# Optimization experiments

Hardware: AMD Instinct MI355X
Metric: run time of the kernel (lower is better)

Reference implementation:

```python
import jax, jax.numpy as jnp
import numpy as np

B, P, D = 64, 128, 128   # clouds, points per cloud, vec_dim
N = B * P                # 8192 nodes
EPS = 1e-5


def _complete_graph_edges():
    # knn_graph with k == total node count => complete graph per cloud (no self loops)
    i = np.arange(P)
    ii, jj = np.meshgrid(i, i, indexing='ij')
    m = ii != jj
    li, lj = ii[m], jj[m]                      # [P*(P-1)] local pairs
    off = (np.arange(B) * P)[:, None]          # cloud offsets
    src = (off + li[None, :]).reshape(-1)      # neighbor index
    dst = (off + lj[None, :]).reshape(-1)      # center index
    return jnp.asarray(src, jnp.int32), jnp.asarray(dst, jnp.int32)


def setup_inputs() -> dict:
    key = jax.random.key(0)
    ks = jax.random.split(key, 4)
    src, dst = _complete_graph_edges()
    return {
        'x': jax.random.normal(ks[0], (N, D), jnp.float32),
        'xyz': jax.random.normal(ks[1], (N, 3), jnp.float32),
        'W_xyz': jax.random.normal(ks[2], (3, D), jnp.float32) * 0.1,
        'bn_gamma': jnp.ones((D,), jnp.float32),
        'bn_beta': jnp.zeros((D,), jnp.float32),
        'W1': jax.random.normal(ks[3], (D, D), jnp.float32) * 0.05,
        'b1': jnp.zeros((D,), jnp.float32),
        'ln_gamma': jnp.ones((D,), jnp.float32),
        'ln_beta': jnp.zeros((D,), jnp.float32),
        'src': src,
        'dst': dst,
    }


def reference(x, xyz, W_xyz, bn_gamma, bn_beta, W1, b1, ln_gamma, ln_beta, src, dst):
    n = x.shape[0]
    rela_xyz = xyz[src] - xyz[dst]                         # [E, 3]
    rela_x = x[src] - x[dst]                               # [E, D]
    dist = jnp.sqrt(jnp.sum(rela_xyz * rela_xyz, axis=-1))  # [E]
    w = jnp.exp(-dist)[:, None]                            # [E, 1]

    # weighted linear + relu, pool by src (global_add_pool over node index)
    h1 = jax.nn.relu((w * rela_x) @ W1 + b1)               # [E, D]
    p1 = jax.ops.segment_sum(h1, src, num_segments=n)      # [N, D]
    mu = jnp.mean(p1, axis=-1, keepdims=True)
    var = jnp.var(p1, axis=-1, keepdims=True)
    x = x + ((p1 - mu) / jnp.sqrt(var + EPS)) * ln_gamma + ln_beta

    # xyz projection branch, BatchNorm1d (training-mode batch stats)
    h2 = jax.nn.relu(rela_xyz @ W_xyz)                     # [E, D]
    p2 = jax.ops.segment_sum(h2, src, num_segments=n)      # [N, D]
    bmu = jnp.mean(p2, axis=0)
    bvar = jnp.var(p2, axis=0)
    x = x + ((p2 - bmu) / jnp.sqrt(bvar + EPS)) * bn_gamma + bn_beta
    return x
```

## Files before the change

### kernel.cpp

```cpp
#include <hip/hip_runtime.h>
#include <stdint.h>

#define EPS 1e-5f
#define N_NODES 8192

typedef __attribute__((ext_vector_type(8))) short short8;
typedef __attribute__((ext_vector_type(4))) float floatx4;
typedef __attribute__((ext_vector_type(2))) float floatx2;
typedef __attribute__((ext_vector_type(4))) unsigned short ushortx4;

__device__ __forceinline__ unsigned short f2bf(float f) {
    uint32_t u = __float_as_uint(f);
    u += 0x7FFFu + ((u >> 16) & 1u);
    return (unsigned short)(u >> 16);
}

__global__ __launch_bounds__(256) void prep_kernel(
    const float* __restrict__ x, const float* __restrict__ W1,
    unsigned short* __restrict__ xb, unsigned short* __restrict__ w1t,
    float* __restrict__ stat_ws)
{
    const int bx = blockIdx.x, tid = threadIdx.x;
    if (bx < 1024) {
        const int base = bx * 1024 + tid * 4;
        floatx4 v = *(const floatx4*)(x + base);
        ushortx4 o = { f2bf(v[0]), f2bf(v[1]), f2bf(v[2]), f2bf(v[3]) };
        *(ushortx4*)(xb + base) = o;
    } else {
        const int b2 = bx - 1024;
        const int n = b2 * 8 + (tid >> 5);
        const int k = (tid & 31) * 4;
#pragma unroll
        for (int e = 0; e < 4; ++e)
            w1t[n * 128 + k + e] = f2bf(W1[(k + e) * 128 + n]);
        if (b2 == 0) {
            floatx4 z = {0.f, 0.f, 0.f, 0.f};
            *(floatx4*)(stat_ws + tid * 4) = z;
        }
    }
}

__global__ __launch_bounds__(64) void gemm_y_kernel(
    const unsigned short* __restrict__ xb, const unsigned short* __restrict__ w1t,
    float* __restrict__ y)
{
    const int lane = threadIdx.x;
    const int ml = lane & 15, q = lane >> 4;
    const int rb = blockIdx.x * 16;

    short8 afrag[4];
#pragma unroll
    for (int c = 0; c < 4; ++c)
        afrag[c] = *(const short8*)(xb + (rb + ml) * 128 + c * 32 + q * 8);

#pragma unroll
    for (int nt = 0; nt < 8; ++nt) {
        floatx4 acc = {0.f, 0.f, 0.f, 0.f};
        const int ncol = nt * 16 + ml;
#pragma unroll
        for (int c = 0; c < 4; ++c) {
            short8 b = *(const short8*)(w1t + ncol * 128 + c * 32 + q * 8);
            acc = __builtin_amdgcn_mfma_f32_16x16x32_bf16(afrag[c], b, acc, 0, 0, 0);
        }
#pragma unroll
        for (int r = 0; r < 4; ++r)
            y[(rb + q * 4 + r) * 128 + ncol] = acc[r];
    }
}

__global__ __launch_bounds__(256, 4) void cloud_main_kernel(
    const float* __restrict__ x, const float* __restrict__ xyz,
    const float* __restrict__ W_xyz, const float* __restrict__ b1,
    const float* __restrict__ ln_gamma, const float* __restrict__ ln_beta,
    const float* __restrict__ y_ws, float* __restrict__ p2_ws,
    float* __restrict__ stat_ws, float* __restrict__ out)
{
    __shared__ float s_xyz[512];
    __shared__ float s_w[1024];
    __shared__ float s_red[2048];
    __shared__ float s_p1[1088];
    __shared__ float s_bn[256];
    __shared__ float s_mu[8];
    __shared__ float s_rs[8];

    const int bx = blockIdx.x;
    const int c = bx & 63, s = bx >> 6;
    const int tid = threadIdx.x;
    const int d = tid & 127, h = tid >> 7;
    const int node0 = c * 128;
    const int i0 = s * 8;

    if (tid < 128) {
        const float* p = xyz + (node0 + tid) * 3;
        s_xyz[tid * 4 + 0] = p[0];
        s_xyz[tid * 4 + 1] = p[1];
        s_xyz[tid * 4 + 2] = p[2];
        s_xyz[tid * 4 + 3] = 0.f;
    }
    __syncthreads();

    for (int e = tid; e < 1024; e += 256) {
        const int j = e >> 3, ii = e & 7, ia = i0 + ii;
        float dx = s_xyz[ia * 4]     - s_xyz[j * 4];
        float dy = s_xyz[ia * 4 + 1] - s_xyz[j * 4 + 1];
        float dz = s_xyz[ia * 4 + 2] - s_xyz[j * 4 + 2];
        s_w[j * 8 + ii] = __expf(-sqrtf(dx * dx + dy * dy + dz * dz));
    }
    __syncthreads();

    const float w0 = W_xyz[d], w1c = W_xyz[128 + d], w2c = W_xyz[256 + d];
    const float b1d = b1[d];
    const floatx2 b1v = {b1d, b1d};
    const floatx2 zv2 = {0.f, 0.f};

    floatx2 yi[4], zi[4], a1[4], a2[4];
#pragma unroll
    for (int r = 0; r < 8; ++r) {
        const int ia = i0 + r;
        yi[r >> 1][r & 1] = y_ws[(node0 + ia) * 128 + d];
        zi[r >> 1][r & 1] = s_xyz[ia * 4] * w0 + s_xyz[ia * 4 + 1] * w1c
                          + s_xyz[ia * 4 + 2] * w2c;
        a1[r >> 1][r & 1] = 0.f;
        a2[r >> 1][r & 1] = 0.f;
    }

    const float* yrow = y_ws + (node0 + h * 64) * 128 + d;
    const float* wp = s_w + h * 64 * 8;
    const float* xp = s_xyz + h * 64 * 4;

#pragma unroll 4
    for (int j = 0; j < 64; ++j) {
        const float yj = yrow[j * 128];
        floatx4 xj = *(const floatx4*)(xp + j * 4);
        const float zj = xj[0] * w0 + xj[1] * w1c + xj[2] * w2c;
        floatx4 wa = *(const floatx4*)(wp + j * 8);
        floatx4 wb = *(const floatx4*)(wp + j * 8 + 4);
        const floatx2 yj2 = {yj, yj}, zj2 = {zj, zj};
        floatx2 wlo = {wa[0], wa[1]}, wmd = {wa[2], wa[3]};
        floatx2 wh0 = {wb[0], wb[1]}, wh1 = {wb[2], wb[3]};
        a1[0] += __builtin_elementwise_max(wlo * (yi[0] - yj2) + b1v, zv2);
        a1[1] += __builtin_elementwise_max(wmd * (yi[1] - yj2) + b1v, zv2);
        a1[2] += __builtin_elementwise_max(wh0 * (yi[2] - yj2) + b1v, zv2);
        a1[3] += __builtin_elementwise_max(wh1 * (yi[3] - yj2) + b1v, zv2);
        a2[0] += __builtin_elementwise_max(zi[0] - zj2, zv2);
        a2[1] += __builtin_elementwise_max(zi[1] - zj2, zv2);
        a2[2] += __builtin_elementwise_max(zi[2] - zj2, zv2);
        a2[3] += __builtin_elementwise_max(zi[3] - zj2, zv2);
    }
    __syncthreads();

    if (h == 1) {
#pragma unroll
        for (int r = 0; r < 8; ++r) {
            s_red[r * 128 + d]        = a1[r >> 1][r & 1];
            s_red[1024 + r * 128 + d] = a2[r >> 1][r & 1];
        }
    }
    __syncthreads();

    if (h == 0) {
        const float selfc = fmaxf(b1d, 0.f);
        float bs = 0.f, bq = 0.f;
#pragma unroll
        for (int r = 0; r < 8; ++r) {
            float v1 = a1[r >> 1][r & 1] + s_red[r * 128 + d] - selfc;
            float v2 = a2[r >> 1][r & 1] + s_red[1024 + r * 128 + d];
            a1[r >> 1][r & 1] = v1;
            a2[r >> 1][r & 1] = v2;
            s_p1[r * 136 + d] = v1;
            bs += v2;
            bq += v2 * v2;
        }
        s_bn[d] = bs;
        s_bn[128 + d] = bq;
    }
    __syncthreads();

    {
        const int ii = tid >> 5, sub = tid & 31;
        floatx4 v = *(const floatx4*)(s_p1 + ii * 136 + sub * 4);
        float ps = v[0] + v[1] + v[2] + v[3];
        float pq = v[0] * v[0] + v[1] * v[1] + v[2] * v[2] + v[3] * v[3];
#pragma unroll
        for (int m = 1; m < 32; m <<= 1) {
            ps += __shfl_xor(ps, m, 64);
            pq += __shfl_xor(pq, m, 64);
        }
        if (sub == 0) {
            float mu = ps * (1.f / 128.f);
            float var = pq * (1.f / 128.f) - mu * mu;
            s_mu[ii] = mu;
            s_rs[ii] = rsqrtf(var + EPS);
        }
    }
    if (tid < 128) {
        const int bank = (s & 3) * 256;
        atomicAdd(stat_ws + bank + d,       s_bn[d]);
        atomicAdd(stat_ws + bank + 128 + d, s_bn[128 + d]);
    }
    __syncthreads();

    if (h == 0) {
        const float lng = ln_gamma[d], lnb = ln_beta[d];
#pragma unroll
        for (int r = 0; r < 8; ++r) {
            const int gi = node0 + i0 + r;
            float o = x[gi * 128 + d] + (a1[r >> 1][r & 1] - s_mu[r]) * s_rs[r] * lng + lnb;
            out[gi * 128 + d] = o;
            p2_ws[gi * 128 + d] = a2[r >> 1][r & 1];
        }
    }
}

__global__ __launch_bounds__(256) void finalize_kernel(
    const float* __restrict__ p2_ws, const float* __restrict__ stat_ws,
    const float* __restrict__ bn_gamma, const float* __restrict__ bn_beta,
    float* __restrict__ out)
{
    __shared__ float sA[128], sB[128];
    const int tid = threadIdx.x;
    if (tid < 128) {
        float sm = 0.f, sq = 0.f;
#pragma unroll
        for (int b = 0; b < 4; ++b) {
            sm += stat_ws[b * 256 + tid];
            sq += stat_ws[b * 256 + 128 + tid];
        }
        float mu = sm * (1.f / 8192.f);
        float var = sq * (1.f / 8192.f) - mu * mu;
        float rs = rsqrtf(var + EPS);
        float A = rs * bn_gamma[tid];
        sA[tid] = A;
        sB[tid] = bn_beta[tid] - mu * A;
    }
    __syncthreads();
    const int base = (blockIdx.x * 256 + tid) * 4;
    const int d0 = base & 127;
    floatx4 p2 = *(const floatx4*)(p2_ws + base);
    floatx4 o  = *(const floatx4*)(out + base);
#pragma unroll
    for (int e = 0; e < 4; ++e)
        o[e] += p2[e] * sA[d0 + e] + sB[d0 + e];
    *(floatx4*)(out + base) = o;
}

extern "C" void kernel_launch(void* const* d_in, const int* in_sizes, int n_in,
                              void* d_out, int out_size, void* d_ws, size_t ws_size,
                              hipStream_t stream) {
    const float* x        = (const float*)d_in[0];
    const float* xyz      = (const float*)d_in[1];
    const float* W_xyz    = (const float*)d_in[2];
    const float* bn_gamma = (const float*)d_in[3];
    const float* bn_beta  = (const float*)d_in[4];
    const float* W1       = (const float*)d_in[5];
    const float* b1       = (const float*)d_in[6];
    const float* ln_gamma = (const float*)d_in[7];
    const float* ln_beta  = (const float*)d_in[8];
    float* out = (float*)d_out;

    float* y_ws    = (float*)d_ws;
    float* p2_ws   = y_ws + N_NODES * 128;
    float* stat_ws = p2_ws + N_NODES * 128;
    unsigned short* xb  = (unsigned short*)(stat_ws + 1024);
    unsigned short* w1t = xb + N_NODES * 128;

    prep_kernel<<<1040, 256, 0, stream>>>(x, W1, xb, w1t, stat_ws);
    gemm_y_kernel<<<512, 64, 0, stream>>>(xb, w1t, y_ws);
    cloud_main_kernel<<<1024, 256, 0, stream>>>(x, xyz, W_xyz, b1, ln_gamma, ln_beta,
                                                y_ws, p2_ws, stat_ws, out);
    finalize_kernel<<<1024, 256, 0, stream>>>(p2_ws, stat_ws, bn_gamma, bn_beta, out);
}
```

Before: 113.9 us.

## Move xyz branch and BN stats before main kernel, fuse finalize and bf16 conversion

```diff
diff --git a/kernel.cpp b/kernel.cpp
--- a/kernel.cpp
+++ b/kernel.cpp
@@ -7,7 +7,6 @@
 typedef __attribute__((ext_vector_type(8))) short short8;
 typedef __attribute__((ext_vector_type(4))) float floatx4;
 typedef __attribute__((ext_vector_type(2))) float floatx2;
-typedef __attribute__((ext_vector_type(4))) unsigned short ushortx4;
 
 __device__ __forceinline__ unsigned short f2bf(float f) {
     uint32_t u = __float_as_uint(f);
@@ -16,72 +15,133 @@
 }
 
 __global__ __launch_bounds__(256) void prep_kernel(
-    const float* __restrict__ x, const float* __restrict__ W1,
-    unsigned short* __restrict__ xb, unsigned short* __restrict__ w1t,
+    const float* __restrict__ W1, unsigned short* __restrict__ w1t,
     float* __restrict__ stat_ws)
 {
-    const int bx = blockIdx.x, tid = threadIdx.x;
-    if (bx < 1024) {
-        const int base = bx * 1024 + tid * 4;
-        floatx4 v = *(const floatx4*)(x + base);
-        ushortx4 o = { f2bf(v[0]), f2bf(v[1]), f2bf(v[2]), f2bf(v[3]) };
-        *(ushortx4*)(xb + base) = o;
+    const int b2 = blockIdx.x, tid = threadIdx.x;
+    const int n = b2 * 8 + (tid >> 5);
+    const int k = (tid & 31) * 4;
+#pragma unroll
+    for (int e = 0; e < 4; ++e)
+        w1t[n * 128 + k + e] = f2bf(W1[(k + e) * 128 + n]);
+    if (b2 == 0) {
+        floatx4 z = {0.f, 0.f, 0.f, 0.f};
+        *(floatx4*)(stat_ws + tid * 4) = z;
+    }
+}
+
+__global__ __launch_bounds__(256, 4) void fused_gemm_p2_kernel(
+    const float* __restrict__ x, const float* __restrict__ xyz,
+    const float* __restrict__ W_xyz, const unsigned short* __restrict__ w1t,
+    float* __restrict__ y_ws, float* __restrict__ p2_ws, float* __restrict__ stat_ws)
+{
+    __shared__ float s_xyz[512];
+    __shared__ float s_red[2048];
+    const int tid = threadIdx.x;
+
+    if (blockIdx.x < 128) {
+        const int w = tid >> 6, lane = tid & 63;
+        const int ml = lane & 15, q = lane >> 4;
+        const int rbw = blockIdx.x * 64 + w * 16;
+
+        short8 afrag[4];
+#pragma unroll
+        for (int c = 0; c < 4; ++c) {
+            const float* px = x + (rbw + ml) * 128 + c * 32 + q * 8;
+            floatx4 v0 = *(const floatx4*)px;
+            floatx4 v1 = *(const floatx4*)(px + 4);
+            short8 a;
+            a[0] = (short)f2bf(v0[0]); a[1] = (short)f2bf(v0[1]);
+            a[2] = (short)f2bf(v0[2]); a[3] = (short)f2bf(v0[3]);
+            a[4] = (short)f2bf(v1[0]); a[5] = (short)f2bf(v1[1]);
+            a[6] = (short)f2bf(v1[2]); a[7] = (short)f2bf(v1[3]);
+            afrag[c] = a;
+        }
+#pragma unroll
+        for (int nt = 0; nt < 8; ++nt) {
+            floatx4 acc = {0.f, 0.f, 0.f, 0.f};
+            const int ncol = nt * 16 + ml;
+#pragma unroll
+            for (int c = 0; c < 4; ++c) {
+                short8 b = *(const short8*)(w1t + ncol * 128 + c * 32 + q * 8);
+                acc = __builtin_amdgcn_mfma_f32_16x16x32_bf16(afrag[c], b, acc, 0, 0, 0);
+            }
+#pragma unroll
+            for (int r = 0; r < 4; ++r)
+                y_ws[(rbw + q * 4 + r) * 128 + ncol] = acc[r];
+        }
     } else {
-        const int b2 = bx - 1024;
-        const int n = b2 * 8 + (tid >> 5);
-        const int k = (tid & 31) * 4;
-#pragma unroll
-        for (int e = 0; e < 4; ++e)
-            w1t[n * 128 + k + e] = f2bf(W1[(k + e) * 128 + n]);
-        if (b2 == 0) {
-            floatx4 z = {0.f, 0.f, 0.f, 0.f};
-            *(floatx4*)(stat_ws + tid * 4) = z;
-        }
-    }
-}
-
-__global__ __launch_bounds__(64) void gemm_y_kernel(
-    const unsigned short* __restrict__ xb, const unsigned short* __restrict__ w1t,
-    float* __restrict__ y)
-{
-    const int lane = threadIdx.x;
-    const int ml = lane & 15, q = lane >> 4;
-    const int rb = blockIdx.x * 16;
-
-    short8 afrag[4];
-#pragma unroll
-    for (int c = 0; c < 4; ++c)
-        afrag[c] = *(const short8*)(xb + (rb + ml) * 128 + c * 32 + q * 8);
-
-#pragma unroll
-    for (int nt = 0; nt < 8; ++nt) {
-        floatx4 acc = {0.f, 0.f, 0.f, 0.f};
-        const int ncol = nt * 16 + ml;
-#pragma unroll
-        for (int c = 0; c < 4; ++c) {
-            short8 b = *(const short8*)(w1t + ncol * 128 + c * 32 + q * 8);
-            acc = __builtin_amdgcn_mfma_f32_16x16x32_bf16(afrag[c], b, acc, 0, 0, 0);
-        }
-#pragma unroll
-        for (int r = 0; r < 4; ++r)
-            y[(rb + q * 4 + r) * 128 + ncol] = acc[r];
+        const int bb = blockIdx.x - 128;
+        const int c = bb >> 3, s = bb & 7;
+        const int d = tid & 127, h = tid >> 7;
+        const int node0 = c * 128, i0 = s * 16;
+
+        if (tid < 128) {
+            const float* p = xyz + (node0 + tid) * 3;
+            s_xyz[tid * 4 + 0] = p[0];
+            s_xyz[tid * 4 + 1] = p[1];
+            s_xyz[tid * 4 + 2] = p[2];
+            s_xyz[tid * 4 + 3] = 0.f;
+        }
+        __syncthreads();
+
+        const float w0 = W_xyz[d], w1c = W_xyz[128 + d], w2c = W_xyz[256 + d];
+        const floatx2 zv2 = {0.f, 0.f};
+        floatx2 zi[8], a2[8];
+#pragma unroll
+        for (int r = 0; r < 16; ++r) {
+            const int ia = i0 + r;
+            zi[r >> 1][r & 1] = s_xyz[ia * 4] * w0 + s_xyz[ia * 4 + 1] * w1c
+                              + s_xyz[ia * 4 + 2] * w2c;
+            a2[r >> 1][r & 1] = 0.f;
+        }
+        const float* xp = s_xyz + h * 256;
+#pragma unroll 4
+        for (int j = 0; j < 64; ++j) {
+            floatx4 xj = *(const floatx4*)(xp + j * 4);
+            const float zj = xj[0] * w0 + xj[1] * w1c + xj[2] * w2c;
+            const floatx2 zj2 = {zj, zj};
+#pragma unroll
+            for (int r = 0; r < 8; ++r)
+                a2[r] += __builtin_elementwise_max(zi[r] - zj2, zv2);
+        }
+        if (h == 1) {
+#pragma unroll
+            for (int r = 0; r < 16; ++r) s_red[r * 128 + d] = a2[r >> 1][r & 1];
+        }
+        __syncthreads();
+        if (h == 0) {
+            float bs = 0.f, bq = 0.f;
+#pragma unroll
+            for (int r = 0; r < 16; ++r) {
+                const float v2 = a2[r >> 1][r & 1] + s_red[r * 128 + d];
+                p2_ws[(node0 + i0 + r) * 128 + d] = v2;
+                bs += v2;
+                bq += v2 * v2;
+            }
+            const int bank = (bb & 3) * 256;
+            atomicAdd(stat_ws + bank + d,       bs);
+            atomicAdd(stat_ws + bank + 128 + d, bq);
+        }
     }
 }
 
 __global__ __launch_bounds__(256, 4) void cloud_main_kernel(
     const float* __restrict__ x, const float* __restrict__ xyz,
-    const float* __restrict__ W_xyz, const float* __restrict__ b1,
-    const float* __restrict__ ln_gamma, const float* __restrict__ ln_beta,
-    const float* __restrict__ y_ws, float* __restrict__ p2_ws,
-    float* __restrict__ stat_ws, float* __restrict__ out)
+    const float* __restrict__ b1, const float* __restrict__ ln_gamma,
+    const float* __restrict__ ln_beta, const float* __restrict__ bn_gamma,
+    const float* __restrict__ bn_beta, const float* __restrict__ y_ws,
+    const float* __restrict__ p2_ws, const float* __restrict__ stat_ws,
+    float* __restrict__ out)
 {
     __shared__ float s_xyz[512];
     __shared__ float s_w[1024];
-    __shared__ float s_red[2048];
+    __shared__ float s_red[1024];
     __shared__ float s_p1[1088];
-    __shared__ float s_bn[256];
     __shared__ float s_mu[8];
     __shared__ float s_rs[8];
+    __shared__ float s_A[128];
+    __shared__ float s_B[128];
 
     const int bx = blockIdx.x;
     const int c = bx & 63, s = bx >> 6;
@@ -96,6 +156,17 @@
         s_xyz[tid * 4 + 1] = p[1];
         s_xyz[tid * 4 + 2] = p[2];
         s_xyz[tid * 4 + 3] = 0.f;
+        float sm = 0.f, sq = 0.f;
+#pragma unroll
+        for (int b = 0; b < 4; ++b) {
+            sm += stat_ws[b * 256 + tid];
+            sq += stat_ws[b * 256 + 128 + tid];
+        }
+        const float mu = sm * (1.f / 8192.f);
+        const float var = sq * (1.f / 8192.f) - mu * mu;
+        const float A = rsqrtf(var + EPS) * bn_gamma[tid];
+        s_A[tid] = A;
+        s_B[tid] = bn_beta[tid] - mu * A;
     }
     __syncthreads();
 
@@ -108,71 +179,48 @@
     }
     __syncthreads();
 
-    const float w0 = W_xyz[d], w1c = W_xyz[128 + d], w2c = W_xyz[256 + d];
     const float b1d = b1[d];
     const floatx2 b1v = {b1d, b1d};
     const floatx2 zv2 = {0.f, 0.f};
 
-    floatx2 yi[4], zi[4], a1[4], a2[4];
+    floatx2 yi[4], a1[4];
 #pragma unroll
     for (int r = 0; r < 8; ++r) {
-        const int ia = i0 + r;
-        yi[r >> 1][r & 1] = y_ws[(node0 + ia) * 128 + d];
-        zi[r >> 1][r & 1] = s_xyz[ia * 4] * w0 + s_xyz[ia * 4 + 1] * w1c
-                          + s_xyz[ia * 4 + 2] * w2c;
+        yi[r >> 1][r & 1] = y_ws[(node0 + i0 + r) * 128 + d];
         a1[r >> 1][r & 1] = 0.f;
-        a2[r >> 1][r & 1] = 0.f;
     }
 
     const float* yrow = y_ws + (node0 + h * 64) * 128 + d;
-    const float* wp = s_w + h * 64 * 8;
-    const float* xp = s_xyz + h * 64 * 4;
+    const float* wp = s_w + h * 512;
 
 #pragma unroll 4
     for (int j = 0; j < 64; ++j) {
         const float yj = yrow[j * 128];
-        floatx4 xj = *(const floatx4*)(xp + j * 4);
-        const float zj = xj[0] * w0 + xj[1] * w1c + xj[2] * w2c;
         floatx4 wa = *(const floatx4*)(wp + j * 8);
         floatx4 wb = *(const floatx4*)(wp + j * 8 + 4);
-        const floatx2 yj2 = {yj, yj}, zj2 = {zj, zj};
+        const floatx2 yj2 = {yj, yj};
         floatx2 wlo = {wa[0], wa[1]}, wmd = {wa[2], wa[3]};
         floatx2 wh0 = {wb[0], wb[1]}, wh1 = {wb[2], wb[3]};
         a1[0] += __builtin_elementwise_max(wlo * (yi[0] - yj2) + b1v, zv2);
         a1[1] += __builtin_elementwise_max(wmd * (yi[1] - yj2) + b1v, zv2);
         a1[2] += __builtin_elementwise_max(wh0 * (yi[2] - yj2) + b1v, zv2);
         a1[3] += __builtin_elementwise_max(wh1 * (yi[3] - yj2) + b1v, zv2);
-        a2[0] += __builtin_elementwise_max(zi[0] - zj2, zv2);
-        a2[1] += __builtin_elementwise_max(zi[1] - zj2, zv2);
-        a2[2] += __builtin_elementwise_max(zi[2] - zj2, zv2);
-        a2[3] += __builtin_elementwise_max(zi[3] - zj2, zv2);
-    }
-    __syncthreads();
+    }
 
     if (h == 1) {
 #pragma unroll
-        for (int r = 0; r < 8; ++r) {
-            s_red[r * 128 + d]        = a1[r >> 1][r & 1];
-            s_red[1024 + r * 128 + d] = a2[r >> 1][r & 1];
-        }
+        for (int r = 0; r < 8; ++r) s_red[r * 128 + d] = a1[r >> 1][r & 1];
     }
     __syncthreads();
 
     if (h == 0) {
         const float selfc = fmaxf(b1d, 0.f);
-        float bs = 0.f, bq = 0.f;
 #pragma unroll
         for (int r = 0; r < 8; ++r) {
-            float v1 = a1[r >> 1][r & 1] + s_red[r * 128 + d] - selfc;
-            float v2 = a2[r >> 1][r & 1] + s_red[1024 + r * 128 + d];
+            const float v1 = a1[r >> 1][r & 1] + s_red[r * 128 + d] - selfc;
             a1[r >> 1][r & 1] = v1;
-            a2[r >> 1][r & 1] = v2;
             s_p1[r * 136 + d] = v1;
-            bs += v2;
-            bq += v2 * v2;
-        }
-        s_bn[d] = bs;
-        s_bn[128 + d] = bq;
+        }
     }
     __syncthreads();
 
@@ -187,61 +235,25 @@
             pq += __shfl_xor(pq, m, 64);
         }
         if (sub == 0) {
-            float mu = ps * (1.f / 128.f);
-            float var = pq * (1.f / 128.f) - mu * mu;
+            const float mu = ps * (1.f / 128.f);
+            const float var = pq * (1.f / 128.f) - mu * mu;
             s_mu[ii] = mu;
             s_rs[ii] = rsqrtf(var + EPS);
         }
     }
-    if (tid < 128) {
-        const int bank = (s & 3) * 256;
-        atomicAdd(stat_ws + bank + d,       s_bn[d]);
-        atomicAdd(stat_ws + bank + 128 + d, s_bn[128 + d]);
-    }
     __syncthreads();
 
     if (h == 0) {
         const float lng = ln_gamma[d], lnb = ln_beta[d];
+        const float A = s_A[d], B = s_B[d];
 #pragma unroll
         for (int r = 0; r < 8; ++r) {
             const int gi = node0 + i0 + r;
-            float o = x[gi * 128 + d] + (a1[r >> 1][r & 1] - s_mu[r]) * s_rs[r] * lng + lnb;
-            out[gi * 128 + d] = o;
-            p2_ws[gi * 128 + d] = a2[r >> 1][r & 1];
-        }
-    }
-}
-
-__global__ __launch_bounds__(256) void finalize_kernel(
-    const float* __restrict__ p2_ws, const float* __restrict__ stat_ws,
-    const float* __restrict__ bn_gamma, const float* __restrict__ bn_beta,
-    float* __restrict__ out)
-{
-    __shared__ float sA[128], sB[128];
-    const int tid = threadIdx.x;
-    if (tid < 128) {
-        float sm = 0.f, sq = 0.f;
-#pragma unroll
-        for (int b = 0; b < 4; ++b) {
-            sm += stat_ws[b * 256 + tid];
-            sq += stat_ws[b * 256 + 128 + tid];
-        }
-        float mu = sm * (1.f / 8192.f);
-        float var = sq * (1.f / 8192.f) - mu * mu;
-        float rs = rsqrtf(var + EPS);
-        float A = rs * bn_gamma[tid];
-        sA[tid] = A;
-        sB[tid] = bn_beta[tid] - mu * A;
-    }
-    __syncthreads();
-    const int base = (blockIdx.x * 256 + tid) * 4;
-    const int d0 = base & 127;
-    floatx4 p2 = *(const floatx4*)(p2_ws + base);
-    floatx4 o  = *(const floatx4*)(out + base);
-#pragma unroll
-    for (int e = 0; e < 4; ++e)
-        o[e] += p2[e] * sA[d0 + e] + sB[d0 + e];
-    *(floatx4*)(out + base) = o;
+            out[gi * 128 + d] = x[gi * 128 + d]
+                + (a1[r >> 1][r & 1] - s_mu[r]) * s_rs[r] * lng + lnb
+                + p2_ws[gi * 128 + d] * A + B;
+        }
+    }
 }
 
 extern "C" void kernel_launch(void* const* d_in, const int* in_sizes, int n_in,
@@ -261,12 +273,11 @@
     float* y_ws    = (float*)d_ws;
     float* p2_ws   = y_ws + N_NODES * 128;
     float* stat_ws = p2_ws + N_NODES * 128;
-    unsigned short* xb  = (unsigned short*)(stat_ws + 1024);
-    unsigned short* w1t = xb + N_NODES * 128;
-
-    prep_kernel<<<1040, 256, 0, stream>>>(x, W1, xb, w1t, stat_ws);
-    gemm_y_kernel<<<512, 64, 0, stream>>>(xb, w1t, y_ws);
-    cloud_main_kernel<<<1024, 256, 0, stream>>>(x, xyz, W_xyz, b1, ln_gamma, ln_beta,
-                                                y_ws, p2_ws, stat_ws, out);
-    finalize_kernel<<<1024, 256, 0, stream>>>(p2_ws, stat_ws, bn_gamma, bn_beta, out);
-}
+    unsigned short* w1t = (unsigned short*)(stat_ws + 1024);
+
+    prep_kernel<<<16, 256, 0, stream>>>(W1, w1t, stat_ws);
+    fused_gemm_p2_kernel<<<640, 256, 0, stream>>>(x, xyz, W_xyz, w1t, y_ws, p2_ws, stat_ws);
+    cloud_main_kernel<<<1024, 256, 0, stream>>>(x, xyz, b1, ln_gamma, ln_beta,
+                                                bn_gamma, bn_beta, y_ws, p2_ws,
+                                                stat_ws, out);
+}
```

Result: faster. 110.8 us (-2.8%).
